# Performance work log

Hardware: AMD Instinct MI355X
Metric: run time of the kernel (lower is better)

Reference implementation:

```python
import jax, jax.numpy as jnp
import numpy as np

B = 8
FF_SIGMA = 1024.0
N_FREQ = 40  # ff_dim // input_dim = 120 // 3


def setup_inputs() -> dict:
    key = jax.random.key(0)
    ks = jax.random.split(key, 12)

    def rn(k, shape, fan_in):
        return jax.random.normal(k, shape, dtype=jnp.float32) * (fan_in ** -0.5)

    return {
        "coord": jax.random.uniform(ks[0], (B, 3), jnp.float32, -1.0, 1.0),
        "feat0": jax.random.normal(ks[1], (B, 256, 16, 16, 30), jnp.float32),
        # 1x1x1 conv weights stored as [in_ch, out_ch]
        "cw1": rn(ks[2], (256, 128), 256), "cb1": jnp.zeros((128,), jnp.float32),
        "cw2": rn(ks[3], (128, 64), 128), "cb2": jnp.zeros((64,), jnp.float32),
        "cw3": rn(ks[4], (64, 32), 64), "cb3": jnp.zeros((32,), jnp.float32),
        # hypernet linear: 32*8*8*15 = 30720 -> c*curr_features = 64*120 = 7680
        "hw": rn(ks[5], (30720, 7680), 30720), "hb": jnp.zeros((7680,), jnp.float32),
        "w1": rn(ks[6], (64, 64), 64), "b1": jnp.zeros((64,), jnp.float32),
        "w2": rn(ks[7], (64, 64), 64), "b2": jnp.zeros((64,), jnp.float32),
        "wo": rn(ks[8], (64, 3), 64), "bo": jnp.zeros((3,), jnp.float32),
    }


def reference(coord, feat0, cw1, cb1, cw2, cb2, cw3, cb3, hw, hb, w1, b1, w2, b2, wo, bo):
    # Fourier features (note: original code does NOT apply sin/cos)
    freqs = jnp.exp(jnp.linspace(0.0, np.log(FF_SIGMA), N_FREQ)).astype(jnp.float32)  # [40]
    z = (coord[:, :, None] * freqs[None, None, :]).reshape(coord.shape[0], -1)  # [B,120]

    # hypernetwork: per-voxel 1x1x1 conv channel-mixing (channel-last layout)
    f = jnp.moveaxis(feat0, 1, -1)                      # [B,16,16,30,256]
    f = jax.nn.relu(f @ cw1 + cb1)                      # [B,16,16,30,128]
    f = jax.nn.relu(f @ cw2 + cb2)                      # [B,16,16,30,64]
    f = jax.nn.relu(f[:, ::2, ::2, ::2, :] @ cw3 + cb3)  # stride-2 kernel-1 conv -> [B,8,8,15,32]
    # torch Flatten order is [B, C, D, H, W]
    f = jnp.moveaxis(f, -1, 1).reshape(f.shape[0], -1)  # [B, 30720]
    w_mod = (f @ hw + hb).reshape(z.shape[0], z.shape[1], -1)  # [B,120,64]

    # modulated layer 0: bmm(z[:,None,:], w_mod).squeeze(1), no activation
    z = jnp.einsum('bf,bfc->bc', z, w_mod)              # [B,64]
    # layers 1,2: Linear + ReLU
    z = jax.nn.relu(z @ w1 + b1)
    z = jax.nn.relu(z @ w2 + b2)
    # final Linear -> output_dim=3
    return z @ wo + bo
```

## Files before the change

kernel.cpp:

```cpp
#include <hip/hip_runtime.h>
#include <hip/hip_bf16.h>

#define DHW (16 * 16 * 30)
#define NWCOL 7680
#define KTOT 30720
#define KSPLIT 96
#define KCH (KTOT / KSPLIT)
#define NBLK (15 * KSPLIT)
#define LN1024_OVER_39 0.17773004629742187f

__global__ __launch_bounds__(512) void k1_conv(
    const float* __restrict__ feat0,
    const float* __restrict__ cw1, const float* __restrict__ cb1,
    const float* __restrict__ cw2, const float* __restrict__ cb2,
    const float* __restrict__ cw3, const float* __restrict__ cb3,
    float* __restrict__ fvecT)
{
    const int yi = blockIdx.x;
    const int zi = blockIdx.y;
    const int b  = blockIdx.z;
    const int t  = threadIdx.x;

    __shared__ float sIn[256][16];
    __shared__ float sW[8192];
    __shared__ float sH1[128][16];
    __shared__ float sH2[64][16];

    {
        const int w  = t & 15;
        const int cg = t >> 4;
        const float* base = feat0 + (size_t)b * 256 * DHW
                            + (2 * zi) * (16 * 30) + (2 * yi) * 30 + 2 * w;
        #pragma unroll
        for (int c0 = 0; c0 < 256; c0 += 32) {
            const int c = c0 + cg;
            sIn[c][w] = (w < 15) ? base[(size_t)c * DHW] : 0.f;
        }
    }

    {
        const int o = t & 127, wq = t >> 7;
        const int w0 = 4 * wq;
        float acc[4];
        const float bv = cb1[o];
        #pragma unroll
        for (int i = 0; i < 4; ++i) acc[i] = bv;

        for (int c0 = 0; c0 < 256; c0 += 64) {
            const float4* src = (const float4*)(cw1 + c0 * 128);
            float4* dst = (float4*)sW;
            #pragma unroll
            for (int p = 0; p < 4; ++p) dst[t + 512 * p] = src[t + 512 * p];
            __syncthreads();
            #pragma unroll 8
            for (int cc = 0; cc < 64; ++cc) {
                const float wv = sW[cc * 128 + o];
                const float4 xi = *(const float4*)&sIn[c0 + cc][w0];
                acc[0] += xi.x * wv;
                acc[1] += xi.y * wv;
                acc[2] += xi.z * wv;
                acc[3] += xi.w * wv;
            }
            __syncthreads();
        }
        #pragma unroll
        for (int i = 0; i < 4; ++i) sH1[o][w0 + i] = fmaxf(acc[i], 0.f);
    }
    __syncthreads();

    {
        const float4* src = (const float4*)cw2;
        float4* dst = (float4*)sW;
        #pragma unroll
        for (int p = 0; p < 4; ++p) dst[t + 512 * p] = src[t + 512 * p];
        __syncthreads();

        const int o = t & 63, q = t >> 6;
        const int w0 = 2 * q;
        float acc[2];
        const float bv = cb2[o];
        acc[0] = bv; acc[1] = bv;
        #pragma unroll 8
        for (int cc = 0; cc < 128; ++cc) {
            const float wv = sW[cc * 64 + o];
            const float2 xi = *(const float2*)&sH1[cc][w0];
            acc[0] += xi.x * wv;
            acc[1] += xi.y * wv;
        }
        sH2[o][w0]     = fmaxf(acc[0], 0.f);
        sH2[o][w0 + 1] = fmaxf(acc[1], 0.f);
    }
    __syncthreads();

    {
        ((float4*)sW)[t] = ((const float4*)cw3)[t];
        __syncthreads();

        const int o = t & 31, w = t >> 5;
        float acc = cb3[o];
        #pragma unroll 8
        for (int cc = 0; cc < 64; ++cc)
            acc += sH2[cc][w] * sW[cc * 32 + o];
        if (w < 15) {
            const int k = ((o * 8 + zi) * 8 + yi) * 15 + w;
            fvecT[(size_t)k * 8 + b] = fmaxf(acc, 0.f);
        }
    }
}

__global__ __launch_bounds__(64) void k2_stream(
    const float* __restrict__ hw,
    const float* __restrict__ fvecT,
    const float* __restrict__ coord,
    float* __restrict__ partial)
{
    __shared__ float zpart[512];
    __shared__ float sF[KCH * 8];
    const int t = threadIdx.x;
    const int kbase = blockIdx.y * KCH;

    #pragma unroll
    for (int r = 0; r < 8; ++r) zpart[t * 8 + r] = 0.f;
    {
        const float4* fsrc = (const float4*)(fvecT + (size_t)kbase * 8);
        float4* fdst = (float4*)sF;
        #pragma unroll
        for (int p = 0; p < 10; ++p) fdst[t + 64 * p] = fsrc[t + 64 * p];
    }
    __syncthreads();

    const int jw = blockIdx.x * 512;
    const int j0 = jw + 4 * t;

    float accA[8][4] = {}, accB[8][4] = {};
    const float* hp = hw + (size_t)kbase * NWCOL + j0;

    #pragma unroll 4
    for (int kk = 0; kk < KCH; ++kk) {
        const float4 hA = *(const float4*)hp;
        const float4 hB = *(const float4*)(hp + 256);
        hp += NWCOL;
        const float4 f0 = *(const float4*)&sF[kk * 8];
        const float4 f1 = *(const float4*)&sF[kk * 8 + 4];
        const float fv[8] = {f0.x, f0.y, f0.z, f0.w, f1.x, f1.y, f1.z, f1.w};
        #pragma unroll
        for (int b = 0; b < 8; ++b) {
            accA[b][0] += fv[b] * hA.x;
            accA[b][1] += fv[b] * hA.y;
            accA[b][2] += fv[b] * hA.z;
            accA[b][3] += fv[b] * hA.w;
            accB[b][0] += fv[b] * hB.x;
            accB[b][1] += fv[b] * hB.y;
            accB[b][2] += fv[b] * hB.z;
            accB[b][3] += fv[b] * hB.w;
        }
    }

    const int fA = 8 * blockIdx.x + (t >> 4);
    const int fB = fA + 4;
    const int i3A = fA / 40, qA = fA - 40 * i3A;
    const int i3B = fB / 40, qB = fB - 40 * i3B;
    const float freqA = __expf((float)qA * LN1024_OVER_39);
    const float freqB = __expf((float)qB * LN1024_OVER_39);
    const int cq = 4 * (t & 15);

    #pragma unroll
    for (int b = 0; b < 8; ++b) {
        const float zvA = coord[b * 3 + i3A] * freqA;
        const float zvB = coord[b * 3 + i3B] * freqB;
        #pragma unroll
        for (int e = 0; e < 4; ++e)
            atomicAdd(&zpart[b * 64 + cq + e],
                      zvA * accA[b][e] + zvB * accB[b][e]);
    }
    __syncthreads();

    const int bid = blockIdx.x + 15 * blockIdx.y;
    float4* pp = (float4*)(partial + (size_t)bid * 512);
    pp[t]      = ((const float4*)zpart)[t];
    pp[t + 64] = ((const float4*)zpart)[t + 64];
}

__global__ __launch_bounds__(256) void k2b_reduce(
    const float* __restrict__ partial, float* __restrict__ z1)
{
    __shared__ float s[256];
    const int t = threadIdx.x;
    const int o = blockIdx.x * 8 + (t & 7);
    float sum = 0.f;
    for (int blk = t >> 3; blk < NBLK; blk += 32)
        sum += partial[(size_t)blk * 512 + o];
    s[t] = sum;
    __syncthreads();
    if (t < 8) {
        float tot = 0.f;
        #pragma unroll
        for (int i = 0; i < 32; ++i) tot += s[t + 8 * i];
        z1[blockIdx.x * 8 + t] = tot;
    }
}

__global__ __launch_bounds__(512) void k3_tail(
    const float* __restrict__ z1acc, const float* __restrict__ coord,
    const float* __restrict__ hb,
    const float* __restrict__ w1, const float* __restrict__ b1,
    const float* __restrict__ w2, const float* __restrict__ b2,
    const float* __restrict__ wo, const float* __restrict__ bo,
    float* __restrict__ out)
{
    __shared__ float shb[7680];
    __shared__ float sw1[4096];
    __shared__ float sw2[4096];
    __shared__ float swo[192];
    __shared__ float sz[8][64];
    __shared__ float s2[8][64];
    __shared__ float sfreq[40];
    __shared__ float sc[24];
    const int t = threadIdx.x;

    #pragma unroll
    for (int p = 0; p < 4; ++p) {
        const int idx = t + 512 * p;
        if (idx < 1920) ((float4*)shb)[idx] = ((const float4*)hb)[idx];
    }
    ((float4*)sw1)[t]       = ((const float4*)w1)[t];
    ((float4*)sw1)[t + 512] = ((const float4*)w1)[t + 512];
    ((float4*)sw2)[t]       = ((const float4*)w2)[t];
    ((float4*)sw2)[t + 512] = ((const float4*)w2)[t + 512];
    if (t < 48) ((float4*)swo)[t] = ((const float4*)wo)[t];
    if (t < 40) sfreq[t] = __expf((float)t * LN1024_OVER_39);
    if (t < 24) sc[t] = coord[t];
    __syncthreads();

    const int b = t >> 6, c = t & 63;

    float a = z1acc[t];
    #pragma unroll
    for (int i = 0; i < 3; ++i) {
        const float cv = sc[b * 3 + i];
        #pragma unroll 8
        for (int q = 0; q < 40; ++q)
            a += cv * sfreq[q] * shb[(i * 40 + q) * 64 + c];
    }
    sz[b][c] = a;
    __syncthreads();

    float a1 = b1[c];
    #pragma unroll 8
    for (int cc = 0; cc < 64; ++cc) a1 += sz[b][cc] * sw1[cc * 64 + c];
    s2[b][c] = fmaxf(a1, 0.f);
    __syncthreads();

    float a2 = b2[c];
    #pragma unroll 8
    for (int cc = 0; cc < 64; ++cc) a2 += s2[b][cc] * sw2[cc * 64 + c];
    sz[b][c] = fmaxf(a2, 0.f);
    __syncthreads();

    if (t < 24) {
        const int bb = t / 3, i = t - bb * 3;
        float o = bo[i];
        #pragma unroll 8
        for (int cc = 0; cc < 64; ++cc) o += sz[bb][cc] * swo[cc * 3 + i];
        out[t] = o;
    }
}

extern "C" void kernel_launch(void* const* d_in, const int* in_sizes, int n_in,
                              void* d_out, int out_size, void* d_ws, size_t ws_size,
                              hipStream_t stream)
{
    const float* coord = (const float*)d_in[0];
    const float* feat0 = (const float*)d_in[1];
    const float* cw1 = (const float*)d_in[2];
    const float* cb1 = (const float*)d_in[3];
    const float* cw2 = (const float*)d_in[4];
    const float* cb2 = (const float*)d_in[5];
    const float* cw3 = (const float*)d_in[6];
    const float* cb3 = (const float*)d_in[7];
    const float* hw  = (const float*)d_in[8];
    const float* hb  = (const float*)d_in[9];
    const float* w1  = (const float*)d_in[10];
    const float* b1  = (const float*)d_in[11];
    const float* w2  = (const float*)d_in[12];
    const float* b2  = (const float*)d_in[13];
    const float* wo  = (const float*)d_in[14];
    const float* bo  = (const float*)d_in[15];
    float* out = (float*)d_out;

    float* fvecT   = (float*)d_ws;
    float* partial = fvecT + (size_t)KTOT * 8;
    float* z1      = partial + (size_t)NBLK * 512;

    k1_conv<<<dim3(8, 8, 8), 512, 0, stream>>>(feat0, cw1, cb1, cw2, cb2,
                                               cw3, cb3, fvecT);
    k2_stream<<<dim3(15, KSPLIT), 64, 0, stream>>>(hw, fvecT, coord, partial);
    k2b_reduce<<<64, 256, 0, stream>>>(partial, z1);
    k3_tail<<<1, 512, 0, stream>>>(z1, coord, hb, w1, b1, w2, b2, wo, bo, out);
}
```

Before: 229.4 us.

## Register-tile conv layers with split-K across thread groups and shared-memory reduction

Restructures the three 1x1x1 conv stages in k1_conv so each thread computes a small output-channel by width register tile and loads weights as vectors. The channel reduction is split across four thread groups, with the partial sums combined through shared memory. This raises arithmetic intensity per LDS load and cuts shared-memory traffic. In exchange it adds extra syncs and a serial reduction done by one quarter of the threads.

```diff
diff --git a/kernel.cpp b/kernel.cpp
--- a/kernel.cpp
+++ b/kernel.cpp
@@ -26,6 +26,11 @@
     __shared__ float sH1[128][16];
     __shared__ float sH2[64][16];
 
+    const int og = t & 31;
+    const int wg = (t >> 5) & 3;
+    const int cs = t >> 7;
+    const int u  = t & 127;
+
     {
         const int w  = t & 15;
         const int cg = t >> 4;
@@ -39,71 +44,156 @@
     }
 
     {
-        const int o = t & 127, wq = t >> 7;
-        const int w0 = 4 * wq;
-        float acc[4];
-        const float bv = cb1[o];
-        #pragma unroll
-        for (int i = 0; i < 4; ++i) acc[i] = bv;
-
+        const int o0 = 4 * og, w0 = 4 * wg;
+        float acc[4][4] = {};
         for (int c0 = 0; c0 < 256; c0 += 64) {
             const float4* src = (const float4*)(cw1 + c0 * 128);
             float4* dst = (float4*)sW;
             #pragma unroll
             for (int p = 0; p < 4; ++p) dst[t + 512 * p] = src[t + 512 * p];
             __syncthreads();
-            #pragma unroll 8
-            for (int cc = 0; cc < 64; ++cc) {
-                const float wv = sW[cc * 128 + o];
+            #pragma unroll 4
+            for (int j = 0; j < 16; ++j) {
+                const int cc = 16 * cs + j;
+                const float4 wv = *(const float4*)&sW[cc * 128 + o0];
                 const float4 xi = *(const float4*)&sIn[c0 + cc][w0];
-                acc[0] += xi.x * wv;
-                acc[1] += xi.y * wv;
-                acc[2] += xi.z * wv;
-                acc[3] += xi.w * wv;
+                acc[0][0] += xi.x * wv.x; acc[0][1] += xi.y * wv.x;
+                acc[0][2] += xi.z * wv.x; acc[0][3] += xi.w * wv.x;
+                acc[1][0] += xi.x * wv.y; acc[1][1] += xi.y * wv.y;
+                acc[1][2] += xi.z * wv.y; acc[1][3] += xi.w * wv.y;
+                acc[2][0] += xi.x * wv.z; acc[2][1] += xi.y * wv.z;
+                acc[2][2] += xi.z * wv.z; acc[2][3] += xi.w * wv.z;
+                acc[3][0] += xi.x * wv.w; acc[3][1] += xi.y * wv.w;
+                acc[3][2] += xi.z * wv.w; acc[3][3] += xi.w * wv.w;
             }
             __syncthreads();
         }
-        #pragma unroll
-        for (int i = 0; i < 4; ++i) sH1[o][w0 + i] = fmaxf(acc[i], 0.f);
-    }
-    __syncthreads();
-
-    {
+        if (cs > 0) {
+            float4* pw = (float4*)&sW[(cs - 1) * 2048 + u * 16];
+            #pragma unroll
+            for (int j = 0; j < 4; ++j) pw[j] = *(const float4*)&acc[j][0];
+        }
+        __syncthreads();
+        if (cs == 0) {
+            #pragma unroll
+            for (int s = 0; s < 3; ++s) {
+                const float4* pr = (const float4*)&sW[s * 2048 + u * 16];
+                #pragma unroll
+                for (int j = 0; j < 4; ++j) {
+                    const float4 v = pr[j];
+                    acc[j][0] += v.x; acc[j][1] += v.y;
+                    acc[j][2] += v.z; acc[j][3] += v.w;
+                }
+            }
+            const float4 bv = *(const float4*)&cb1[o0];
+            const float bb[4] = {bv.x, bv.y, bv.z, bv.w};
+            #pragma unroll
+            for (int j = 0; j < 4; ++j) {
+                float4 r;
+                r.x = fmaxf(acc[j][0] + bb[j], 0.f);
+                r.y = fmaxf(acc[j][1] + bb[j], 0.f);
+                r.z = fmaxf(acc[j][2] + bb[j], 0.f);
+                r.w = fmaxf(acc[j][3] + bb[j], 0.f);
+                *(float4*)&sH1[o0 + j][w0] = r;
+            }
+        }
+        __syncthreads();
+    }
+
+    {
+        const int o0 = 2 * og, w0 = 4 * wg;
         const float4* src = (const float4*)cw2;
         float4* dst = (float4*)sW;
         #pragma unroll
         for (int p = 0; p < 4; ++p) dst[t + 512 * p] = src[t + 512 * p];
         __syncthreads();
 
-        const int o = t & 63, q = t >> 6;
-        const int w0 = 2 * q;
-        float acc[2];
-        const float bv = cb2[o];
-        acc[0] = bv; acc[1] = bv;
-        #pragma unroll 8
-        for (int cc = 0; cc < 128; ++cc) {
-            const float wv = sW[cc * 64 + o];
-            const float2 xi = *(const float2*)&sH1[cc][w0];
-            acc[0] += xi.x * wv;
-            acc[1] += xi.y * wv;
-        }
-        sH2[o][w0]     = fmaxf(acc[0], 0.f);
-        sH2[o][w0 + 1] = fmaxf(acc[1], 0.f);
-    }
-    __syncthreads();
-
-    {
-        ((float4*)sW)[t] = ((const float4*)cw3)[t];
-        __syncthreads();
-
-        const int o = t & 31, w = t >> 5;
-        float acc = cb3[o];
-        #pragma unroll 8
-        for (int cc = 0; cc < 64; ++cc)
-            acc += sH2[cc][w] * sW[cc * 32 + o];
-        if (w < 15) {
-            const int k = ((o * 8 + zi) * 8 + yi) * 15 + w;
-            fvecT[(size_t)k * 8 + b] = fmaxf(acc, 0.f);
+        float acc[2][4] = {};
+        #pragma unroll 4
+        for (int j = 0; j < 32; ++j) {
+            const int cc = 32 * cs + j;
+            const float2 wv = *(const float2*)&sW[cc * 64 + o0];
+            const float4 xi = *(const float4*)&sH1[cc][w0];
+            acc[0][0] += xi.x * wv.x; acc[0][1] += xi.y * wv.x;
+            acc[0][2] += xi.z * wv.x; acc[0][3] += xi.w * wv.x;
+            acc[1][0] += xi.x * wv.y; acc[1][1] += xi.y * wv.y;
+            acc[1][2] += xi.z * wv.y; acc[1][3] += xi.w * wv.y;
+        }
+        __syncthreads();
+
+        if (cs > 0) {
+            float4* pw = (float4*)&sW[(cs - 1) * 1024 + u * 8];
+            pw[0] = *(const float4*)&acc[0][0];
+            pw[1] = *(const float4*)&acc[1][0];
+        }
+        ((float4*)&sW[4096])[t] = ((const float4*)cw3)[t];
+        __syncthreads();
+
+        if (cs == 0) {
+            #pragma unroll
+            for (int s = 0; s < 3; ++s) {
+                const float4* pr = (const float4*)&sW[s * 1024 + u * 8];
+                const float4 v0 = pr[0], v1 = pr[1];
+                acc[0][0] += v0.x; acc[0][1] += v0.y;
+                acc[0][2] += v0.z; acc[0][3] += v0.w;
+                acc[1][0] += v1.x; acc[1][1] += v1.y;
+                acc[1][2] += v1.z; acc[1][3] += v1.w;
+            }
+            const float2 bv = *(const float2*)&cb2[o0];
+            float4 r0, r1;
+            r0.x = fmaxf(acc[0][0] + bv.x, 0.f);
+            r0.y = fmaxf(acc[0][1] + bv.x, 0.f);
+            r0.z = fmaxf(acc[0][2] + bv.x, 0.f);
+            r0.w = fmaxf(acc[0][3] + bv.x, 0.f);
+            r1.x = fmaxf(acc[1][0] + bv.y, 0.f);
+            r1.y = fmaxf(acc[1][1] + bv.y, 0.f);
+            r1.z = fmaxf(acc[1][2] + bv.y, 0.f);
+            r1.w = fmaxf(acc[1][3] + bv.y, 0.f);
+            *(float4*)&sH2[o0][w0]     = r0;
+            *(float4*)&sH2[o0 + 1][w0] = r1;
+        }
+        __syncthreads();
+    }
+
+    {
+        const int og3 = t & 15, wg3 = (t >> 4) & 7, cs3 = t >> 7;
+        const int o0 = 2 * og3, w0 = 2 * wg3;
+        const int u3 = t & 127;
+        float acc[2][2] = {};
+        #pragma unroll 4
+        for (int j = 0; j < 16; ++j) {
+            const int cc = 16 * cs3 + j;
+            const float2 wv = *(const float2*)&sW[4096 + cc * 32 + o0];
+            const float2 xi = *(const float2*)&sH2[cc][w0];
+            acc[0][0] += xi.x * wv.x; acc[0][1] += xi.y * wv.x;
+            acc[1][0] += xi.x * wv.y; acc[1][1] += xi.y * wv.y;
+        }
+        if (cs3 > 0) {
+            float4 v;
+            v.x = acc[0][0]; v.y = acc[0][1]; v.z = acc[1][0]; v.w = acc[1][1];
+            *(float4*)&sW[(cs3 - 1) * 512 + u3 * 4] = v;
+        }
+        __syncthreads();
+        if (cs3 == 0) {
+            #pragma unroll
+            for (int s = 0; s < 3; ++s) {
+                const float4 v = *(const float4*)&sW[s * 512 + u3 * 4];
+                acc[0][0] += v.x; acc[0][1] += v.y;
+                acc[1][0] += v.z; acc[1][1] += v.w;
+            }
+            const float2 bv = *(const float2*)&cb3[o0];
+            #pragma unroll
+            for (int oj = 0; oj < 2; ++oj) {
+                const int kbase = (((o0 + oj) * 8 + zi) * 8 + yi) * 15;
+                const float bj = oj ? bv.y : bv.x;
+                #pragma unroll
+                for (int wj = 0; wj < 2; ++wj) {
+                    const int w = w0 + wj;
+                    if (w < 15)
+                        fvecT[(size_t)(kbase + w) * 8 + b] =
+                            fmaxf(acc[oj][wj] + bj, 0.f);
+                }
+            }
         }
     }
 }
```

Result: faster. 220.7 us (-3.8%).
